# Performance work log

Measured on AMD Instinct MI355X. Metric: run time of the kernel, lower is better.

## Reference

```python
import jax, jax.numpy as jnp
import numpy as np

D_MODEL = 1472
N_HEADS = 6
D_KV = 64
INNER = N_HEADS * D_KV
NUM_BUCKETS = 32
MAX_DIST = 128


def _relative_position_bucket(relative_position, bidirectional=True,
                              num_buckets=NUM_BUCKETS, max_distance=MAX_DIST):
    ret = jnp.zeros_like(relative_position)
    if bidirectional:
        num_buckets //= 2
        ret = ret + (relative_position > 0).astype(jnp.int32) * num_buckets
        rel = jnp.abs(relative_position)
    else:
        rel = -jnp.minimum(relative_position, 0)
    max_exact = num_buckets // 2
    is_small = rel < max_exact
    rel_f = jnp.maximum(rel, 1).astype(jnp.float32)
    large = max_exact + (
        jnp.log(rel_f / max_exact) / np.log(max_distance / max_exact)
        * (num_buckets - max_exact)
    ).astype(jnp.int32)
    large = jnp.minimum(large, num_buckets - 1)
    return ret + jnp.where(is_small, rel, large)


def _position_bias(q_len, k_len, rel_bias):
    # rel_bias: [num_buckets, n_heads]
    ctx = jnp.arange(q_len)[:, None]
    mem = jnp.arange(k_len)[None, :]
    buckets = _relative_position_bucket(mem - ctx, bidirectional=True)
    values = rel_bias[buckets]                 # [Q, K, H]
    return jnp.transpose(values, (2, 0, 1))[None]  # [1, H, Q, K]


def setup_inputs() -> dict:
    key = jax.random.key(0)
    ks = jax.random.split(key, 8)
    B, S = 4, 2048
    scale = 0.02
    return {
        "kv_sequences": jax.random.normal(ks[0], (B, S, D_MODEL), jnp.float32),
        "q_sequences": jax.random.normal(ks[1], (B, S, D_MODEL), jnp.float32),
        "mask": jnp.zeros((B, 1, S, S), jnp.float32),
        "WQ": jax.random.normal(ks[2], (D_MODEL, INNER), jnp.float32) * scale,
        "WK": jax.random.normal(ks[3], (D_MODEL, INNER), jnp.float32) * scale,
        "WV": jax.random.normal(ks[4], (D_MODEL, INNER), jnp.float32) * scale,
        "WO": jax.random.normal(ks[5], (INNER, D_MODEL), jnp.float32) * scale,
        "rel_bias": jax.random.normal(ks[6], (NUM_BUCKETS, N_HEADS), jnp.float32) * scale,
    }


def reference(kv_sequences, q_sequences, mask, WQ, WK, WV, WO, rel_bias):
    B, Kl, _ = kv_sequences.shape
    Ql = q_sequences.shape[1]
    # projections -> [B, H, L, d_kv]
    q = (q_sequences @ WQ).reshape(B, Ql, N_HEADS, D_KV).transpose(0, 2, 1, 3)
    k = (kv_sequences @ WK).reshape(B, Kl, N_HEADS, D_KV).transpose(0, 2, 1, 3)
    v = (kv_sequences @ WV).reshape(B, Kl, N_HEADS, D_KV).transpose(0, 2, 1, 3)
    # T5-style: no 1/sqrt(d) scaling
    logits = jnp.einsum("bhqd,bhkd->bhqk", q, k)
    logits = logits + _position_bias(Ql, Kl, rel_bias)
    logits = logits + mask
    attn = jax.nn.softmax(logits.astype(jnp.float32), axis=-1).astype(logits.dtype)
    out = jnp.einsum("bhqk,bhkd->bhqd", attn, v)
    out = out.transpose(0, 2, 1, 3).reshape(B, Ql, INNER)
    return out @ WO
```

## Files before the change

### kernel.cpp

```cpp
#include <hip/hip_runtime.h>
#include <hip/hip_fp16.h>
#include <cstdint>

#define DM    1472
#define NH    6
#define DKV   64
#define INNER 384
#define BATCH 4
#define SEQ   2048
#define LOG2E 1.4426950408889634f

typedef __attribute__((ext_vector_type(8))) _Float16 half8;
typedef __attribute__((ext_vector_type(4))) _Float16 half4;
typedef __attribute__((ext_vector_type(4))) float f32x4;

__device__ __forceinline__ int swz64(int row, int b)  { return b ^ (((row >> 1) & 3) << 4); }

__device__ __forceinline__ void gload16(const void* g, const void* l) {
  __builtin_amdgcn_global_load_lds((const __attribute__((address_space(1))) void*)g,
                                   (__attribute__((address_space(3))) void*)l, 16, 0, 0);
}

__global__ void prep_weights(const float* __restrict__ WQ, const float* __restrict__ WK,
                             const float* __restrict__ WV, const float* __restrict__ WO,
                             _Float16* __restrict__ WqT, _Float16* __restrict__ WkT,
                             _Float16* __restrict__ WvT, _Float16* __restrict__ WoT) {
  int idx = blockIdx.x * blockDim.x + threadIdx.x;
  const int per = DM * INNER;
  if (idx >= 4 * per) return;
  int which = idx / per;
  int i = idx - which * per;
  if (which < 3) {
    const float* W = which == 0 ? WQ : (which == 1 ? WK : WV);
    _Float16* T = which == 0 ? WqT : (which == 1 ? WkT : WvT);
    int k = i / INNER, n = i - (i / INNER) * INNER;
    T[(size_t)n * DM + k] = (_Float16)W[i];
  } else {
    int k = i / DM, n = i - (i / DM) * DM;
    WoT[(size_t)n * INNER + k] = (_Float16)WO[i];
  }
}

__global__ void prep_bias(const float* __restrict__ rel_bias, float* __restrict__ biasS) {
  int idx = blockIdx.x * blockDim.x + threadIdx.x;
  const int TOT = NH * 4 * 4104;
  if (idx >= TOT) return;
  int h = idx / (4 * 4104);
  int rem = idx - h * 4 * 4104;
  int cc = rem / 4104;
  int i = rem - cc * 4104;
  int j = i + cc; if (j > 4094) j = 4094;
  int d = j - 2047;
  int ret = d > 0 ? 16 : 0;
  int a = d < 0 ? -d : d;
  int bucket;
  if (a < 8) bucket = ret + a;
  else {
    int large;
    if      (a >= 91) large = 15;
    else if (a >= 64) large = 14;
    else if (a >= 46) large = 13;
    else if (a >= 32) large = 12;
    else if (a >= 23) large = 11;
    else if (a >= 16) large = 10;
    else if (a >= 12) large = 9;
    else              large = 8;
    bucket = ret + large;
  }
  biasS[idx] = rel_bias[bucket * NH + h] * LOG2E;
}

__global__ __launch_bounds__(256) void proj_gemm(
    const float* __restrict__ Xq, const float* __restrict__ Xkv,
    const _Float16* __restrict__ WqT, const _Float16* __restrict__ WkvT,
    _Float16* __restrict__ Qo, _Float16* __restrict__ Ko, _Float16* __restrict__ Vto) {
  const int bm = blockIdx.x, by = blockIdx.y;
  const bool isQ = by < 3;
  const float* __restrict__ X = isQ ? Xq : Xkv;
  const _Float16* __restrict__ WT = isQ ? (WqT + (size_t)by * 128 * DM)
                                        : (WkvT + (size_t)(by - 3) * 128 * DM);

  __shared__ alignas(16) float    As[2][128 * 32];
  __shared__ alignas(16) _Float16 Bs[2][128 * 32];

  const int tid = threadIdx.x;
  const int lane = tid & 63, wave = tid >> 6;
  const int wm = wave >> 1, wn = wave & 1;
  const int l15 = lane & 15, lg = lane >> 4;

  f32x4 acc[4][4] = {};

  const int aoff = 4 * ((lane & 7) ^ (lane >> 3));
  const float* asrc[4];
#pragma unroll
  for (int c = 0; c < 4; ++c)
    asrc[c] = X + (size_t)(bm * 128 + (wave * 4 + c) * 8 + (lane >> 3)) * DM + aoff;
  const int boff = 8 * ((lane & 3) ^ ((lane >> 3) & 3));
  const _Float16* bsrc[2];
#pragma unroll
  for (int c = 0; c < 2; ++c)
    bsrc[c] = WT + (size_t)((wave * 2 + c) * 16 + (lane >> 2)) * DM + boff;

  const int NT = DM / 32;

#pragma unroll
  for (int c = 0; c < 4; ++c)
    gload16(asrc[c], (const char*)&As[0][0] + (wave * 4 + c) * 1024);
#pragma unroll
  for (int c = 0; c < 2; ++c)
    gload16(bsrc[c], (const char*)&Bs[0][0] + (wave * 2 + c) * 1024);
  __syncthreads();

  for (int t = 0; t < NT; ++t) {
    if (t + 1 < NT) {
      const int nb = (t + 1) & 1;
      const int kf = (t + 1) * 32;
#pragma unroll
      for (int c = 0; c < 4; ++c)
        gload16(asrc[c] + kf, (const char*)&As[nb][0] + (wave * 4 + c) * 1024);
#pragma unroll
      for (int c = 0; c < 2; ++c)
        gload16(bsrc[c] + kf, (const char*)&Bs[nb][0] + (wave * 2 + c) * 1024);
    }

    const char* Ab = (const char*)&As[t & 1][0];
    const char* Bb = (const char*)&Bs[t & 1][0];
    half8 af[4], bf[4];
#pragma unroll
    for (int m = 0; m < 4; ++m) {
      int r = wm * 64 + m * 16 + l15;
      int s = (r & 7) << 4;
      f32x4 x0 = *(const f32x4*)(Ab + r * 128 + ((lg * 32) ^ s));
      f32x4 x1 = *(const f32x4*)(Ab + r * 128 + ((lg * 32 + 16) ^ s));
      half8 h;
#pragma unroll
      for (int j = 0; j < 4; ++j) { h[j] = (_Float16)x0[j]; h[4 + j] = (_Float16)x1[j]; }
      af[m] = h;
    }
#pragma unroll
    for (int n = 0; n < 4; ++n) {
      int r = wn * 64 + n * 16 + l15;
      bf[n] = *(const half8*)(Bb + r * 64 + ((lg * 16) ^ (((r >> 1) & 3) << 4)));
    }

    __builtin_amdgcn_s_setprio(1);
#pragma unroll
    for (int m = 0; m < 4; ++m)
#pragma unroll
      for (int n = 0; n < 4; ++n)
        acc[m][n] = __builtin_amdgcn_mfma_f32_16x16x32_f16(af[m], bf[n], acc[m][n], 0, 0, 0);
    __builtin_amdgcn_s_setprio(0);

    __syncthreads();
  }

#pragma unroll
  for (int m = 0; m < 4; ++m)
#pragma unroll
    for (int n = 0; n < 4; ++n)
#pragma unroll
      for (int r = 0; r < 4; ++r) {
        int gm = bm * 128 + wm * 64 + m * 16 + lg * 4 + r;
        int gnl = wn * 64 + n * 16 + l15;
        int b = gm >> 11, s = gm & 2047;
        float av = acc[m][n][r];
        if (isQ) {
          int gn = by * 128 + gnl;
          int h = gn >> 6, dd = gn & 63;
          Qo[((size_t)(b * NH + h) * SEQ + s) * DKV + dd] = (_Float16)(av * LOG2E);
        } else {
          int gn = (by - 3) * 128 + gnl;
          if (gn < INNER) {
            int h = gn >> 6, dd = gn & 63;
            Ko[((size_t)(b * NH + h) * SEQ + s) * DKV + dd] = (_Float16)av;
          } else {
            int gnv = gn - INNER;
            int h = gnv >> 6, dd = gnv & 63;
            Vto[((size_t)(b * NH + h) * DKV + dd) * SEQ + s] = (_Float16)av;
          }
        }
      }
}

__global__ __launch_bounds__(256, 3) void attn_kernel(
    const _Float16* __restrict__ Q, const _Float16* __restrict__ K, const _Float16* __restrict__ Vt,
    const float* __restrict__ biasS, const float* __restrict__ mask, _Float16* __restrict__ AO) {
  const int bid = blockIdx.x;
  const int g = (bid & 7) * 96 + (bid >> 3);
  const int bh = g >> 5, qb = g & 31;
  const int b = bh / NH, h = bh - b * NH;
  const int q0 = qb * 64;
  const int tid = threadIdx.x, lane = tid & 63, wave = tid >> 6;
  const int l15 = lane & 15, lg = lane >> 4;
  const int NT = SEQ / 64;

  __shared__ alignas(16) _Float16 Ks[3][64 * 64];
  __shared__ alignas(16) _Float16 Vs[2][64 * 64];
  __shared__ alignas(16) _Float16 Ps[4][16 * 72];

  const size_t bhS = (size_t)bh * SEQ;
  const int qq = q0 + wave * 16 + l15;

  const _Float16* Qbase = Q + (bhS + q0 + wave * 16) * DKV;
  half8 qf0 = *(const half8*)(Qbase + (size_t)l15 * DKV + lg * 8);
  half8 qf1 = *(const half8*)(Qbase + (size_t)l15 * DKV + 32 + lg * 8);

  const float* maskrow = mask + (size_t)b * SEQ * SEQ + (size_t)qq * SEQ + lg * 4;
  const int c = (3 - l15) & 3;
  const float* bbase = biasS + (size_t)(h * 4 + c) * 4104 + (lg * 4 - qq + 2047 - c);

  float m_r = -1e30f, l_acc = 0.f;
  f32x4 oacc[4] = {};

  const int rl = lane >> 3;
  const int sw = ((lane & 7) ^ rl) * 8;
  const _Float16* Kd0 = K + (bhS + wave * 16 + rl) * DKV + sw;
  const _Float16* Kd1 = Kd0 + 8 * DKV;
  const _Float16* Vd0 = Vt + ((size_t)bh * DKV + wave * 16 + rl) * SEQ + sw;
  const _Float16* Vd1 = Vd0 + 8 * SEQ;
  char* KsB = (char*)&Ks[0][0];
  char* VsB = (char*)&Vs[0][0];
  char* PsB = (char*)&Ps[wave][0];
  const int dmaLds = wave * 2048;

  gload16(Kd0, KsB + dmaLds);
  gload16(Kd1, KsB + dmaLds + 1024);
  gload16(Kd0 + 64 * DKV, KsB + 8192 + dmaLds);
  gload16(Kd1 + 64 * DKV, KsB + 8192 + dmaLds + 1024);
  gload16(Vd0, VsB + dmaLds);
  gload16(Vd1, VsB + dmaLds + 1024);

  f32x4 mA[4], mB[4];
#pragma unroll
  for (int nf = 0; nf < 4; ++nf) mA[nf] = *(const f32x4*)(maskrow + nf * 16);

  __syncthreads();

  f32x4 sA[4] = {}, sB[4] = {};
  __builtin_amdgcn_s_setprio(1);
#pragma unroll
  for (int nf = 0; nf < 4; ++nf) {
    int kr = nf * 16 + l15;
    const char* rb = KsB + kr * 128;
    half8 kf0 = *(const half8*)(rb + ((lg ^ (kr & 7)) << 4));
    half8 kf1 = *(const half8*)(rb + (((4 + lg) ^ (kr & 7)) << 4));
    sA[nf] = __builtin_amdgcn_mfma_f32_16x16x32_f16(kf0, qf0, sA[nf], 0, 0, 0);
    sA[nf] = __builtin_amdgcn_mfma_f32_16x16x32_f16(kf1, qf1, sA[nf], 0, 0, 0);
  }
  __builtin_amdgcn_s_setprio(0);

  auto body = [&](int t, f32x4 (&sC)[4], f32x4 (&sN)[4], f32x4 (&mC)[4], f32x4 (&mN)[4]) {
    const int nt1 = t + 1, nt2 = t + 2;
    if (nt2 < NT) {
      char* kb = KsB + (nt2 % 3) * 8192 + dmaLds;
      gload16(Kd0 + (size_t)nt2 * 64 * DKV, kb);
      gload16(Kd1 + (size_t)nt2 * 64 * DKV, kb + 1024);
    }
    if (nt1 < NT) {
      char* vb_ = VsB + (nt1 & 1) * 8192 + dmaLds;
      gload16(Vd0 + nt1 * 64, vb_);
      gload16(Vd1 + nt1 * 64, vb_ + 1024);
#pragma unroll
      for (int nf = 0; nf < 4; ++nf)
        mN[nf] = *(const f32x4*)(maskrow + nt1 * 64 + nf * 16);
    }

#pragma unroll
    for (int nf = 0; nf < 4; ++nf) sN[nf] = (f32x4){0.f, 0.f, 0.f, 0.f};
    if (nt1 < NT) {
      const char* Kb = KsB + (nt1 % 3) * 8192;
      __builtin_amdgcn_s_setprio(1);
#pragma unroll
      for (int nf = 0; nf < 4; ++nf) {
        int kr = nf * 16 + l15;
        const char* rb = Kb + kr * 128;
        half8 kf0 = *(const half8*)(rb + ((lg ^ (kr & 7)) << 4));
        half8 kf1 = *(const half8*)(rb + (((4 + lg) ^ (kr & 7)) << 4));
        sN[nf] = __builtin_amdgcn_mfma_f32_16x16x32_f16(kf0, qf0, sN[nf], 0, 0, 0);
        sN[nf] = __builtin_amdgcn_mfma_f32_16x16x32_f16(kf1, qf1, sN[nf], 0, 0, 0);
      }
      __builtin_amdgcn_s_setprio(0);
    }

    float fm[4];
#pragma unroll
    for (int nf = 0; nf < 4; ++nf) {
      f32x4 bv = *(const f32x4*)(bbase + t * 64 + nf * 16);
#pragma unroll
      for (int r = 0; r < 4; ++r)
        sC[nf][r] = sC[nf][r] + bv[r] + mC[nf][r] * LOG2E;
      fm[nf] = fmaxf(fmaxf(sC[nf][0], sC[nf][1]), fmaxf(sC[nf][2], sC[nf][3]));
    }
    float mx = fmaxf(fmaxf(fm[0], fm[1]), fmaxf(fm[2], fm[3]));
    mx = fmaxf(mx, __shfl_xor(mx, 16));
    mx = fmaxf(mx, __shfl_xor(mx, 32));

    if (!__all(mx <= m_r + 8.0f)) {
      float mnew = fmaxf(m_r, mx);
      float sc_ = __builtin_amdgcn_exp2f(m_r - mnew);
      m_r = mnew;
      l_acc *= sc_;
      f32x4 scv;
#pragma unroll
      for (int r = 0; r < 4; ++r) scv[r] = __shfl(sc_, lg * 4 + r);
#pragma unroll
      for (int df = 0; df < 4; ++df) oacc[df] *= scv;
    }

    float rs = 0.f;
#pragma unroll
    for (int nf = 0; nf < 4; ++nf) {
      half4 ph;
#pragma unroll
      for (int r = 0; r < 4; ++r) {
        float p = __builtin_amdgcn_exp2f(sC[nf][r] - m_r);
        rs += p;
        ph[r] = (_Float16)p;
      }
      *(half4*)(PsB + l15 * 144 + nf * 32 + lg * 8) = ph;
    }
    l_acc += rs;

    const char* Vb = VsB + (t & 1) * 8192;
    __builtin_amdgcn_s_setprio(1);
#pragma unroll
    for (int ks = 0; ks < 2; ++ks) {
      half8 pa = *(const half8*)(PsB + l15 * 144 + ks * 64 + lg * 16);
#pragma unroll
      for (int df = 0; df < 4; ++df) {
        int vr = df * 16 + l15;
        half8 vv = *(const half8*)(Vb + vr * 128 + (((ks * 4 + lg) ^ (vr & 7)) << 4));
        oacc[df] = __builtin_amdgcn_mfma_f32_16x16x32_f16(pa, vv, oacc[df], 0, 0, 0);
      }
    }
    __builtin_amdgcn_s_setprio(0);

    __syncthreads();
  };

  for (int tt = 0; tt < NT / 2; ++tt) {
    body(2 * tt,     sA, sB, mA, mB);
    body(2 * tt + 1, sB, sA, mB, mA);
  }

  l_acc += __shfl_xor(l_acc, 16);
  l_acc += __shfl_xor(l_acc, 32);
  f32x4 lv;
#pragma unroll
  for (int r = 0; r < 4; ++r) lv[r] = __shfl(l_acc, lg * 4 + r);
#pragma unroll
  for (int df = 0; df < 4; ++df) {
    int dd = df * 16 + l15;
#pragma unroll
    for (int r = 0; r < 4; ++r) {
      int qrow = q0 + wave * 16 + lg * 4 + r;
      AO[((size_t)(b * SEQ + qrow)) * INNER + h * DKV + dd] = (_Float16)(oacc[df][r] / lv[r]);
    }
  }
}

__global__ __launch_bounds__(256) void out_gemm(
    const _Float16* __restrict__ A, const _Float16* __restrict__ BT, float* __restrict__ C) {
  __shared__ alignas(16) _Float16 As[2][128 * 32];
  __shared__ alignas(16) _Float16 Bs[2][64 * 32];

  const int tid = threadIdx.x, lane = tid & 63, wave = tid >> 6;
  const int wm = wave >> 1, wn = wave & 1;
  const int bm = blockIdx.x, bn = blockIdx.y;
  const int l15 = lane & 15, lg = lane >> 4;

  f32x4 acc[4][2] = {};

  const int rl4 = (lane >> 2) & 3;
  const int soff = ((lane & 3) ^ rl4) * 8;
  const _Float16* ad0 = A + (size_t)(bm * 128 + (wave * 2) * 16 + (lane >> 2)) * INNER + soff;
  const _Float16* ad1 = ad0 + (size_t)16 * INNER;
  const _Float16* bd0 = BT + (size_t)(bn * 64 + wave * 16 + (lane >> 2)) * INNER + soff;
  char* AsB = (char*)&As[0][0];
  char* BsB = (char*)&Bs[0][0];
  const int aLds = wave * 2048;
  const int bLds = wave * 1024;

  const int NT = INNER / 32;

  gload16(ad0, AsB + aLds);
  gload16(ad1, AsB + aLds + 1024);
  gload16(bd0, BsB + bLds);
  __syncthreads();

  for (int t = 0; t < NT; ++t) {
    if (t + 1 < NT) {
      const int nb = (t + 1) & 1;
      const int kf = (t + 1) * 32;
      gload16(ad0 + kf, AsB + nb * 8192 + aLds);
      gload16(ad1 + kf, AsB + nb * 8192 + aLds + 1024);
      gload16(bd0 + kf, BsB + nb * 4096 + bLds);
    }

    const char* Ab = AsB + (t & 1) * 8192;
    const char* Bb = BsB + (t & 1) * 4096;
    half8 af[4], bf[2];
#pragma unroll
    for (int m = 0; m < 4; ++m) {
      int r = wm * 64 + m * 16 + l15;
      af[m] = *(const half8*)(Ab + r * 64 + (((lg ^ (r & 3))) << 4));
    }
#pragma unroll
    for (int n = 0; n < 2; ++n) {
      int r = wn * 32 + n * 16 + l15;
      bf[n] = *(const half8*)(Bb + r * 64 + (((lg ^ (r & 3))) << 4));
    }
    __builtin_amdgcn_s_setprio(1);
#pragma unroll
    for (int m = 0; m < 4; ++m)
#pragma unroll
      for (int n = 0; n < 2; ++n)
        acc[m][n] = __builtin_amdgcn_mfma_f32_16x16x32_f16(af[m], bf[n], acc[m][n], 0, 0, 0);
    __builtin_amdgcn_s_setprio(0);

    __syncthreads();
  }

#pragma unroll
  for (int m = 0; m < 4; ++m)
#pragma unroll
    for (int n = 0; n < 2; ++n)
#pragma unroll
      for (int r = 0; r < 4; ++r) {
        int gm = bm * 128 + wm * 64 + m * 16 + lg * 4 + r;
        int gn = bn * 64 + wn * 32 + n * 16 + l15;
        C[(size_t)gm * DM + gn] = acc[m][n][r];
      }
}

extern "C" void kernel_launch(void* const* d_in, const int* in_sizes, int n_in,
                              void* d_out, int out_size, void* d_ws, size_t ws_size,
                              hipStream_t stream) {
  const float* kv   = (const float*)d_in[0];
  const float* qs   = (const float*)d_in[1];
  const float* mask = (const float*)d_in[2];
  const float* WQ   = (const float*)d_in[3];
  const float* WK   = (const float*)d_in[4];
  const float* WV   = (const float*)d_in[5];
  const float* WO   = (const float*)d_in[6];
  const float* rb   = (const float*)d_in[7];
  float* out = (float*)d_out;
  char* ws = (char*)d_ws;

  const size_t WT_BYTES  = (size_t)INNER * DM * 2;
  const size_t QKV_BYTES = (size_t)BATCH * NH * SEQ * DKV * 2;
  _Float16* WqT = (_Float16*)(ws);
  _Float16* WkT = (_Float16*)(ws + WT_BYTES);
  _Float16* WvT = (_Float16*)(ws + 2 * WT_BYTES);
  _Float16* WoT = (_Float16*)(ws + 3 * WT_BYTES);
  _Float16* Qh  = (_Float16*)(ws + 4 * WT_BYTES);
  _Float16* Kh  = (_Float16*)(ws + 4 * WT_BYTES + QKV_BYTES);
  _Float16* Vth = (_Float16*)(ws + 4 * WT_BYTES + 2 * QKV_BYTES);
  _Float16* AO  = (_Float16*)(ws + 4 * WT_BYTES + 3 * QKV_BYTES);
  float* biasS  = (float*)(ws + 4 * WT_BYTES + 4 * QKV_BYTES);

  hipLaunchKernelGGL(prep_weights, dim3((4 * DM * INNER + 255) / 256), dim3(256), 0, stream,
                     WQ, WK, WV, WO, WqT, WkT, WvT, WoT);
  hipLaunchKernelGGL(prep_bias, dim3((NH * 4 * 4104 + 255) / 256), dim3(256), 0, stream, rb, biasS);
  hipLaunchKernelGGL(proj_gemm, dim3(64, 9), dim3(256), 0, stream,
                     qs, kv, WqT, WkT, Qh, Kh, Vth);
  hipLaunchKernelGGL(attn_kernel, dim3(768), dim3(256), 0, stream,
                     Qh, Kh, Vth, biasS, mask, AO);
  hipLaunchKernelGGL(out_gemm, dim3(64, 23), dim3(256), 0, stream, AO, WoT, out);
}
```

Baseline: 193.7 us.

## Split attention over two key halves with atomic-counter merge of partials

Turns the attention kernel into a split-K (flash-decoding style) variant: each (batch, head, query-block) is handled by two workgroups, each over half the keys. Each writes unnormalized output plus max/sum partials to workspace, and the last finisher, found via an atomic counter, merges them. This doubles the grid from 768 to 1536 blocks to fill more CUs. It also simplifies the pipeline to plain double buffering without the software-pipelined QK, raises the occupancy hint to 4, and swizzles the P buffer instead of padding it. The costs are extra global traffic for partials, a memset launch, and a possibly less overlapped inner loop.

```diff
diff --git a/kernel.cpp b/kernel.cpp
--- a/kernel.cpp
+++ b/kernel.cpp
@@ -13,8 +13,6 @@
 typedef __attribute__((ext_vector_type(8))) _Float16 half8;
 typedef __attribute__((ext_vector_type(4))) _Float16 half4;
 typedef __attribute__((ext_vector_type(4))) float f32x4;
-
-__device__ __forceinline__ int swz64(int row, int b)  { return b ^ (((row >> 1) & 3) << 4); }
 
 __device__ __forceinline__ void gload16(const void* g, const void* l) {
   __builtin_amdgcn_global_load_lds((const __attribute__((address_space(1))) void*)g,
@@ -182,21 +180,33 @@
       }
 }
 
-__global__ __launch_bounds__(256, 3) void attn_kernel(
+template <int KHALVES>
+__global__ __launch_bounds__(256, 4) void attn_kernel(
     const _Float16* __restrict__ Q, const _Float16* __restrict__ K, const _Float16* __restrict__ Vt,
-    const float* __restrict__ biasS, const float* __restrict__ mask, _Float16* __restrict__ AO) {
+    const float* __restrict__ biasS, const float* __restrict__ mask, _Float16* __restrict__ AO,
+    float* __restrict__ Opart, float* __restrict__ MLpart, int* __restrict__ cnt) {
   const int bid = blockIdx.x;
-  const int g = (bid & 7) * 96 + (bid >> 3);
-  const int bh = g >> 5, qb = g & 31;
+  int pair, half;
+  if constexpr (KHALVES == 2) {
+    int g = (bid & 7) * 192 + (bid >> 3);
+    pair = g >> 1; half = g & 1;
+  } else {
+    pair = (bid & 7) * 96 + (bid >> 3);
+    half = 0;
+  }
+  const int bh = pair >> 5, qb = pair & 31;
   const int b = bh / NH, h = bh - b * NH;
   const int q0 = qb * 64;
+  const int k0 = half * (SEQ / KHALVES);
+  const int NT = (SEQ / KHALVES) / 64;
+
   const int tid = threadIdx.x, lane = tid & 63, wave = tid >> 6;
   const int l15 = lane & 15, lg = lane >> 4;
-  const int NT = SEQ / 64;
-
-  __shared__ alignas(16) _Float16 Ks[3][64 * 64];
+
+  __shared__ alignas(16) _Float16 Ks[2][64 * 64];
   __shared__ alignas(16) _Float16 Vs[2][64 * 64];
-  __shared__ alignas(16) _Float16 Ps[4][16 * 72];
+  __shared__ alignas(16) _Float16 Ps[4][16 * 64];
+  __shared__ int lastFlag;
 
   const size_t bhS = (size_t)bh * SEQ;
   const int qq = q0 + wave * 16 + l15;
@@ -205,18 +215,18 @@
   half8 qf0 = *(const half8*)(Qbase + (size_t)l15 * DKV + lg * 8);
   half8 qf1 = *(const half8*)(Qbase + (size_t)l15 * DKV + 32 + lg * 8);
 
-  const float* maskrow = mask + (size_t)b * SEQ * SEQ + (size_t)qq * SEQ + lg * 4;
+  const float* maskrow = mask + (size_t)b * SEQ * SEQ + (size_t)qq * SEQ + k0 + lg * 4;
   const int c = (3 - l15) & 3;
-  const float* bbase = biasS + (size_t)(h * 4 + c) * 4104 + (lg * 4 - qq + 2047 - c);
+  const float* bbase = biasS + (size_t)(h * 4 + c) * 4104 + (k0 + lg * 4 - qq + 2047 - c);
 
   float m_r = -1e30f, l_acc = 0.f;
   f32x4 oacc[4] = {};
 
   const int rl = lane >> 3;
   const int sw = ((lane & 7) ^ rl) * 8;
-  const _Float16* Kd0 = K + (bhS + wave * 16 + rl) * DKV + sw;
+  const _Float16* Kd0 = K + (bhS + k0 + wave * 16 + rl) * DKV + sw;
   const _Float16* Kd1 = Kd0 + 8 * DKV;
-  const _Float16* Vd0 = Vt + ((size_t)bh * DKV + wave * 16 + rl) * SEQ + sw;
+  const _Float16* Vd0 = Vt + ((size_t)bh * DKV + wave * 16 + rl) * SEQ + k0 + sw;
   const _Float16* Vd1 = Vd0 + 8 * SEQ;
   char* KsB = (char*)&Ks[0][0];
   char* VsB = (char*)&Vs[0][0];
@@ -225,71 +235,43 @@
 
   gload16(Kd0, KsB + dmaLds);
   gload16(Kd1, KsB + dmaLds + 1024);
-  gload16(Kd0 + 64 * DKV, KsB + 8192 + dmaLds);
-  gload16(Kd1 + 64 * DKV, KsB + 8192 + dmaLds + 1024);
   gload16(Vd0, VsB + dmaLds);
   gload16(Vd1, VsB + dmaLds + 1024);
-
-  f32x4 mA[4], mB[4];
-#pragma unroll
-  for (int nf = 0; nf < 4; ++nf) mA[nf] = *(const f32x4*)(maskrow + nf * 16);
-
   __syncthreads();
 
-  f32x4 sA[4] = {}, sB[4] = {};
-  __builtin_amdgcn_s_setprio(1);
-#pragma unroll
-  for (int nf = 0; nf < 4; ++nf) {
-    int kr = nf * 16 + l15;
-    const char* rb = KsB + kr * 128;
-    half8 kf0 = *(const half8*)(rb + ((lg ^ (kr & 7)) << 4));
-    half8 kf1 = *(const half8*)(rb + (((4 + lg) ^ (kr & 7)) << 4));
-    sA[nf] = __builtin_amdgcn_mfma_f32_16x16x32_f16(kf0, qf0, sA[nf], 0, 0, 0);
-    sA[nf] = __builtin_amdgcn_mfma_f32_16x16x32_f16(kf1, qf1, sA[nf], 0, 0, 0);
-  }
-  __builtin_amdgcn_s_setprio(0);
-
-  auto body = [&](int t, f32x4 (&sC)[4], f32x4 (&sN)[4], f32x4 (&mC)[4], f32x4 (&mN)[4]) {
-    const int nt1 = t + 1, nt2 = t + 2;
-    if (nt2 < NT) {
-      char* kb = KsB + (nt2 % 3) * 8192 + dmaLds;
-      gload16(Kd0 + (size_t)nt2 * 64 * DKV, kb);
-      gload16(Kd1 + (size_t)nt2 * 64 * DKV, kb + 1024);
-    }
-    if (nt1 < NT) {
-      char* vb_ = VsB + (nt1 & 1) * 8192 + dmaLds;
-      gload16(Vd0 + nt1 * 64, vb_);
-      gload16(Vd1 + nt1 * 64, vb_ + 1024);
-#pragma unroll
-      for (int nf = 0; nf < 4; ++nf)
-        mN[nf] = *(const f32x4*)(maskrow + nt1 * 64 + nf * 16);
-    }
-
-#pragma unroll
-    for (int nf = 0; nf < 4; ++nf) sN[nf] = (f32x4){0.f, 0.f, 0.f, 0.f};
-    if (nt1 < NT) {
-      const char* Kb = KsB + (nt1 % 3) * 8192;
-      __builtin_amdgcn_s_setprio(1);
-#pragma unroll
-      for (int nf = 0; nf < 4; ++nf) {
-        int kr = nf * 16 + l15;
-        const char* rb = Kb + kr * 128;
-        half8 kf0 = *(const half8*)(rb + ((lg ^ (kr & 7)) << 4));
-        half8 kf1 = *(const half8*)(rb + (((4 + lg) ^ (kr & 7)) << 4));
-        sN[nf] = __builtin_amdgcn_mfma_f32_16x16x32_f16(kf0, qf0, sN[nf], 0, 0, 0);
-        sN[nf] = __builtin_amdgcn_mfma_f32_16x16x32_f16(kf1, qf1, sN[nf], 0, 0, 0);
-      }
-      __builtin_amdgcn_s_setprio(0);
-    }
-
-    float fm[4];
+  for (int t = 0; t < NT; ++t) {
+    if (t + 1 < NT) {
+      const int nb = (t + 1) & 1;
+      gload16(Kd0 + (size_t)(t + 1) * 64 * DKV, KsB + nb * 8192 + dmaLds);
+      gload16(Kd1 + (size_t)(t + 1) * 64 * DKV, KsB + nb * 8192 + dmaLds + 1024);
+      gload16(Vd0 + (t + 1) * 64, VsB + nb * 8192 + dmaLds);
+      gload16(Vd1 + (t + 1) * 64, VsB + nb * 8192 + dmaLds + 1024);
+    }
+    const char* Kb = KsB + (t & 1) * 8192;
+    const char* Vb = VsB + (t & 1) * 8192;
+
+    f32x4 sacc[4] = {};
+    __builtin_amdgcn_s_setprio(1);
+#pragma unroll
+    for (int nf = 0; nf < 4; ++nf) {
+      int kr = nf * 16 + l15;
+      const char* rb = Kb + kr * 128;
+      half8 kf0 = *(const half8*)(rb + ((lg ^ (kr & 7)) << 4));
+      half8 kf1 = *(const half8*)(rb + (((4 + lg) ^ (kr & 7)) << 4));
+      sacc[nf] = __builtin_amdgcn_mfma_f32_16x16x32_f16(kf0, qf0, sacc[nf], 0, 0, 0);
+      sacc[nf] = __builtin_amdgcn_mfma_f32_16x16x32_f16(kf1, qf1, sacc[nf], 0, 0, 0);
+    }
+    __builtin_amdgcn_s_setprio(0);
+
+    float sv[4][4], fm[4];
 #pragma unroll
     for (int nf = 0; nf < 4; ++nf) {
       f32x4 bv = *(const f32x4*)(bbase + t * 64 + nf * 16);
+      f32x4 mv = *(const f32x4*)(maskrow + t * 64 + nf * 16);
 #pragma unroll
       for (int r = 0; r < 4; ++r)
-        sC[nf][r] = sC[nf][r] + bv[r] + mC[nf][r] * LOG2E;
-      fm[nf] = fmaxf(fmaxf(sC[nf][0], sC[nf][1]), fmaxf(sC[nf][2], sC[nf][3]));
+        sv[nf][r] = sacc[nf][r] + bv[r] + mv[r] * LOG2E;
+      fm[nf] = fmaxf(fmaxf(sv[nf][0], sv[nf][1]), fmaxf(sv[nf][2], sv[nf][3]));
     }
     float mx = fmaxf(fmaxf(fm[0], fm[1]), fmaxf(fm[2], fm[3]));
     mx = fmaxf(mx, __shfl_xor(mx, 16));
@@ -313,48 +295,89 @@
       half4 ph;
 #pragma unroll
       for (int r = 0; r < 4; ++r) {
-        float p = __builtin_amdgcn_exp2f(sC[nf][r] - m_r);
+        float p = __builtin_amdgcn_exp2f(sv[nf][r] - m_r);
         rs += p;
         ph[r] = (_Float16)p;
       }
-      *(half4*)(PsB + l15 * 144 + nf * 32 + lg * 8) = ph;
+      *(half4*)(PsB + l15 * 128 + ((((nf << 1) + (lg >> 1)) ^ (l15 & 7)) << 4) + ((lg & 1) << 3)) = ph;
     }
     l_acc += rs;
 
-    const char* Vb = VsB + (t & 1) * 8192;
     __builtin_amdgcn_s_setprio(1);
 #pragma unroll
     for (int ks = 0; ks < 2; ++ks) {
-      half8 pa = *(const half8*)(PsB + l15 * 144 + ks * 64 + lg * 16);
+      half8 pa = *(const half8*)(PsB + l15 * 128 + ((((ks << 2) + lg) ^ (l15 & 7)) << 4));
 #pragma unroll
       for (int df = 0; df < 4; ++df) {
         int vr = df * 16 + l15;
-        half8 vv = *(const half8*)(Vb + vr * 128 + (((ks * 4 + lg) ^ (vr & 7)) << 4));
+        half8 vv = *(const half8*)(Vb + vr * 128 + ((((ks << 2) + lg) ^ (vr & 7)) << 4));
         oacc[df] = __builtin_amdgcn_mfma_f32_16x16x32_f16(pa, vv, oacc[df], 0, 0, 0);
       }
     }
     __builtin_amdgcn_s_setprio(0);
 
     __syncthreads();
-  };
-
-  for (int tt = 0; tt < NT / 2; ++tt) {
-    body(2 * tt,     sA, sB, mA, mB);
-    body(2 * tt + 1, sB, sA, mB, mA);
   }
 
   l_acc += __shfl_xor(l_acc, 16);
   l_acc += __shfl_xor(l_acc, 32);
-  f32x4 lv;
-#pragma unroll
-  for (int r = 0; r < 4; ++r) lv[r] = __shfl(l_acc, lg * 4 + r);
-#pragma unroll
-  for (int df = 0; df < 4; ++df) {
-    int dd = df * 16 + l15;
+
+  if constexpr (KHALVES == 1) {
+    f32x4 lv;
+#pragma unroll
+    for (int r = 0; r < 4; ++r) lv[r] = __shfl(l_acc, lg * 4 + r);
+#pragma unroll
+    for (int df = 0; df < 4; ++df) {
+      int dd = df * 16 + l15;
+#pragma unroll
+      for (int r = 0; r < 4; ++r) {
+        int qrow = q0 + wave * 16 + lg * 4 + r;
+        AO[((size_t)(b * SEQ + qrow)) * INNER + h * DKV + dd] = (_Float16)(oacc[df][r] / lv[r]);
+      }
+    }
+  } else {
+    float* Og = Opart + (size_t)(pair * 2 + half) * 4096;
+#pragma unroll
+    for (int df = 0; df < 4; ++df)
+      *(f32x4*)(Og + (df * 16 + l15) * 64 + wave * 16 + lg * 4) = oacc[df];
+    float* Ml = MLpart + (size_t)pair * 256 + half * 128;
+    if (lane < 16) {
+      Ml[wave * 16 + l15] = m_r;
+      Ml[64 + wave * 16 + l15] = l_acc;
+    }
+    __syncthreads();
+    if (tid == 0) {
+      __threadfence();
+      lastFlag = atomicAdd(&cnt[pair], 1);
+    }
+    __syncthreads();
+    if (lastFlag == 0) return;
+    __threadfence();
+
+    const float* Oo = Opart + (size_t)(pair * 2 + (half ^ 1)) * 4096;
+    const float* Mo = MLpart + (size_t)pair * 256 + (half ^ 1) * 128;
+    float a[4], ao[4], Lr[4];
 #pragma unroll
     for (int r = 0; r < 4; ++r) {
-      int qrow = q0 + wave * 16 + lg * 4 + r;
-      AO[((size_t)(b * SEQ + qrow)) * INNER + h * DKV + dd] = (_Float16)(oacc[df][r] / lv[r]);
+      int ql = wave * 16 + lg * 4 + r;
+      float mreg = __shfl(m_r, lg * 4 + r);
+      float lreg = __shfl(l_acc, lg * 4 + r);
+      float mo = Mo[ql], lo = Mo[64 + ql];
+      float mm = fmaxf(mreg, mo);
+      a[r]  = __builtin_amdgcn_exp2f(mreg - mm);
+      ao[r] = __builtin_amdgcn_exp2f(mo - mm);
+      Lr[r] = a[r] * lreg + ao[r] * lo;
+    }
+#pragma unroll
+    for (int df = 0; df < 4; ++df) {
+      f32x4 Ov = *(const f32x4*)(Oo + (df * 16 + l15) * 64 + wave * 16 + lg * 4);
+      int dd = df * 16 + l15;
+#pragma unroll
+      for (int r = 0; r < 4; ++r) {
+        int qrow = q0 + wave * 16 + lg * 4 + r;
+        float v = (a[r] * oacc[df][r] + ao[r] * Ov[r]) / Lr[r];
+        AO[((size_t)(b * SEQ + qrow)) * INNER + h * DKV + dd] = (_Float16)v;
+      }
     }
   }
 }
@@ -458,13 +481,26 @@
   _Float16* Vth = (_Float16*)(ws + 4 * WT_BYTES + 2 * QKV_BYTES);
   _Float16* AO  = (_Float16*)(ws + 4 * WT_BYTES + 3 * QKV_BYTES);
   float* biasS  = (float*)(ws + 4 * WT_BYTES + 4 * QKV_BYTES);
+  size_t off = 4 * WT_BYTES + 4 * QKV_BYTES + (size_t)NH * 4 * 4104 * 4;
+  off = (off + 255) & ~(size_t)255;
+  float* Opart  = (float*)(ws + off);
+  float* MLpart = (float*)(ws + off + (size_t)1536 * 4096 * 4);
+  int*   cnt    = (int*)(ws + off + (size_t)1536 * 4096 * 4 + (size_t)768 * 256 * 4);
+  const size_t needed = off + (size_t)1536 * 4096 * 4 + (size_t)768 * 256 * 4 + 768 * 4;
+  const bool split = ws_size >= needed;
 
   hipLaunchKernelGGL(prep_weights, dim3((4 * DM * INNER + 255) / 256), dim3(256), 0, stream,
                      WQ, WK, WV, WO, WqT, WkT, WvT, WoT);
   hipLaunchKernelGGL(prep_bias, dim3((NH * 4 * 4104 + 255) / 256), dim3(256), 0, stream, rb, biasS);
   hipLaunchKernelGGL(proj_gemm, dim3(64, 9), dim3(256), 0, stream,
                      qs, kv, WqT, WkT, Qh, Kh, Vth);
-  hipLaunchKernelGGL(attn_kernel, dim3(768), dim3(256), 0, stream,
-                     Qh, Kh, Vth, biasS, mask, AO);
+  if (split) {
+    hipMemsetAsync(cnt, 0, 768 * sizeof(int), stream);
+    hipLaunchKernelGGL((attn_kernel<2>), dim3(1536), dim3(256), 0, stream,
+                       Qh, Kh, Vth, biasS, mask, AO, Opart, MLpart, cnt);
+  } else {
+    hipLaunchKernelGGL((attn_kernel<1>), dim3(768), dim3(256), 0, stream,
+                       Qh, Kh, Vth, biasS, mask, AO, nullptr, nullptr, nullptr);
+  }
   hipLaunchKernelGGL(out_gemm, dim3(64, 23), dim3(256), 0, stream, AO, WoT, out);
 }
```

New measurement: 367.8 us. +89.9%, slower.

## Simplify attention pipeline to double-buffered K/V and raise occupancy to four blocks

Applied to the files above, without the earlier changes.

Drops the software-pipelined QK^T (computing the next tile's scores during the current softmax) and the triple-buffered K ring. K and V now share a plain double buffer and the mask is loaded inline each tile. Freeing registers and LDS allows launch bounds of 4 blocks per SM, and the P scratch uses an XOR swizzle instead of padding. The trade is losing intra-wave overlap of MFMA and softmax plus exposed mask-load latency, in exchange for more waves to hide latency.

```diff
diff --git a/kernel.cpp b/kernel.cpp
--- a/kernel.cpp
+++ b/kernel.cpp
@@ -13,8 +13,6 @@
 typedef __attribute__((ext_vector_type(8))) _Float16 half8;
 typedef __attribute__((ext_vector_type(4))) _Float16 half4;
 typedef __attribute__((ext_vector_type(4))) float f32x4;
-
-__device__ __forceinline__ int swz64(int row, int b)  { return b ^ (((row >> 1) & 3) << 4); }
 
 __device__ __forceinline__ void gload16(const void* g, const void* l) {
   __builtin_amdgcn_global_load_lds((const __attribute__((address_space(1))) void*)g,
@@ -182,7 +180,7 @@
       }
 }
 
-__global__ __launch_bounds__(256, 3) void attn_kernel(
+__global__ __launch_bounds__(256, 4) void attn_kernel(
     const _Float16* __restrict__ Q, const _Float16* __restrict__ K, const _Float16* __restrict__ Vt,
     const float* __restrict__ biasS, const float* __restrict__ mask, _Float16* __restrict__ AO) {
   const int bid = blockIdx.x;
@@ -190,13 +188,14 @@
   const int bh = g >> 5, qb = g & 31;
   const int b = bh / NH, h = bh - b * NH;
   const int q0 = qb * 64;
+  const int NT = SEQ / 64;
+
   const int tid = threadIdx.x, lane = tid & 63, wave = tid >> 6;
   const int l15 = lane & 15, lg = lane >> 4;
-  const int NT = SEQ / 64;
-
-  __shared__ alignas(16) _Float16 Ks[3][64 * 64];
+
+  __shared__ alignas(16) _Float16 Ks[2][64 * 64];
   __shared__ alignas(16) _Float16 Vs[2][64 * 64];
-  __shared__ alignas(16) _Float16 Ps[4][16 * 72];
+  __shared__ alignas(16) _Float16 Ps[4][16 * 64];
 
   const size_t bhS = (size_t)bh * SEQ;
   const int qq = q0 + wave * 16 + l15;
@@ -225,71 +224,43 @@
 
   gload16(Kd0, KsB + dmaLds);
   gload16(Kd1, KsB + dmaLds + 1024);
-  gload16(Kd0 + 64 * DKV, KsB + 8192 + dmaLds);
-  gload16(Kd1 + 64 * DKV, KsB + 8192 + dmaLds + 1024);
   gload16(Vd0, VsB + dmaLds);
   gload16(Vd1, VsB + dmaLds + 1024);
-
-  f32x4 mA[4], mB[4];
-#pragma unroll
-  for (int nf = 0; nf < 4; ++nf) mA[nf] = *(const f32x4*)(maskrow + nf * 16);
-
   __syncthreads();
 
-  f32x4 sA[4] = {}, sB[4] = {};
-  __builtin_amdgcn_s_setprio(1);
-#pragma unroll
-  for (int nf = 0; nf < 4; ++nf) {
-    int kr = nf * 16 + l15;
-    const char* rb = KsB + kr * 128;
-    half8 kf0 = *(const half8*)(rb + ((lg ^ (kr & 7)) << 4));
-    half8 kf1 = *(const half8*)(rb + (((4 + lg) ^ (kr & 7)) << 4));
-    sA[nf] = __builtin_amdgcn_mfma_f32_16x16x32_f16(kf0, qf0, sA[nf], 0, 0, 0);
-    sA[nf] = __builtin_amdgcn_mfma_f32_16x16x32_f16(kf1, qf1, sA[nf], 0, 0, 0);
-  }
-  __builtin_amdgcn_s_setprio(0);
-
-  auto body = [&](int t, f32x4 (&sC)[4], f32x4 (&sN)[4], f32x4 (&mC)[4], f32x4 (&mN)[4]) {
-    const int nt1 = t + 1, nt2 = t + 2;
-    if (nt2 < NT) {
-      char* kb = KsB + (nt2 % 3) * 8192 + dmaLds;
-      gload16(Kd0 + (size_t)nt2 * 64 * DKV, kb);
-      gload16(Kd1 + (size_t)nt2 * 64 * DKV, kb + 1024);
-    }
-    if (nt1 < NT) {
-      char* vb_ = VsB + (nt1 & 1) * 8192 + dmaLds;
-      gload16(Vd0 + nt1 * 64, vb_);
-      gload16(Vd1 + nt1 * 64, vb_ + 1024);
-#pragma unroll
-      for (int nf = 0; nf < 4; ++nf)
-        mN[nf] = *(const f32x4*)(maskrow + nt1 * 64 + nf * 16);
-    }
-
-#pragma unroll
-    for (int nf = 0; nf < 4; ++nf) sN[nf] = (f32x4){0.f, 0.f, 0.f, 0.f};
-    if (nt1 < NT) {
-      const char* Kb = KsB + (nt1 % 3) * 8192;
-      __builtin_amdgcn_s_setprio(1);
-#pragma unroll
-      for (int nf = 0; nf < 4; ++nf) {
-        int kr = nf * 16 + l15;
-        const char* rb = Kb + kr * 128;
-        half8 kf0 = *(const half8*)(rb + ((lg ^ (kr & 7)) << 4));
-        half8 kf1 = *(const half8*)(rb + (((4 + lg) ^ (kr & 7)) << 4));
-        sN[nf] = __builtin_amdgcn_mfma_f32_16x16x32_f16(kf0, qf0, sN[nf], 0, 0, 0);
-        sN[nf] = __builtin_amdgcn_mfma_f32_16x16x32_f16(kf1, qf1, sN[nf], 0, 0, 0);
-      }
-      __builtin_amdgcn_s_setprio(0);
-    }
-
-    float fm[4];
+  for (int t = 0; t < NT; ++t) {
+    if (t + 1 < NT) {
+      const int nb = (t + 1) & 1;
+      gload16(Kd0 + (size_t)(t + 1) * 64 * DKV, KsB + nb * 8192 + dmaLds);
+      gload16(Kd1 + (size_t)(t + 1) * 64 * DKV, KsB + nb * 8192 + dmaLds + 1024);
+      gload16(Vd0 + (t + 1) * 64, VsB + nb * 8192 + dmaLds);
+      gload16(Vd1 + (t + 1) * 64, VsB + nb * 8192 + dmaLds + 1024);
+    }
+    const char* Kb = KsB + (t & 1) * 8192;
+    const char* Vb = VsB + (t & 1) * 8192;
+
+    f32x4 sacc[4] = {};
+    __builtin_amdgcn_s_setprio(1);
+#pragma unroll
+    for (int nf = 0; nf < 4; ++nf) {
+      int kr = nf * 16 + l15;
+      const char* rb = Kb + kr * 128;
+      half8 kf0 = *(const half8*)(rb + ((lg ^ (kr & 7)) << 4));
+      half8 kf1 = *(const half8*)(rb + (((4 + lg) ^ (kr & 7)) << 4));
+      sacc[nf] = __builtin_amdgcn_mfma_f32_16x16x32_f16(kf0, qf0, sacc[nf], 0, 0, 0);
+      sacc[nf] = __builtin_amdgcn_mfma_f32_16x16x32_f16(kf1, qf1, sacc[nf], 0, 0, 0);
+    }
+    __builtin_amdgcn_s_setprio(0);
+
+    float sv[4][4], fm[4];
 #pragma unroll
     for (int nf = 0; nf < 4; ++nf) {
       f32x4 bv = *(const f32x4*)(bbase + t * 64 + nf * 16);
+      f32x4 mv = *(const f32x4*)(maskrow + t * 64 + nf * 16);
 #pragma unroll
       for (int r = 0; r < 4; ++r)
-        sC[nf][r] = sC[nf][r] + bv[r] + mC[nf][r] * LOG2E;
-      fm[nf] = fmaxf(fmaxf(sC[nf][0], sC[nf][1]), fmaxf(sC[nf][2], sC[nf][3]));
+        sv[nf][r] = sacc[nf][r] + bv[r] + mv[r] * LOG2E;
+      fm[nf] = fmaxf(fmaxf(sv[nf][0], sv[nf][1]), fmaxf(sv[nf][2], sv[nf][3]));
     }
     float mx = fmaxf(fmaxf(fm[0], fm[1]), fmaxf(fm[2], fm[3]));
     mx = fmaxf(mx, __shfl_xor(mx, 16));
@@ -313,34 +284,28 @@
       half4 ph;
 #pragma unroll
       for (int r = 0; r < 4; ++r) {
-        float p = __builtin_amdgcn_exp2f(sC[nf][r] - m_r);
+        float p = __builtin_amdgcn_exp2f(sv[nf][r] - m_r);
         rs += p;
         ph[r] = (_Float16)p;
       }
-      *(half4*)(PsB + l15 * 144 + nf * 32 + lg * 8) = ph;
+      *(half4*)(PsB + l15 * 128 + ((((nf << 1) + (lg >> 1)) ^ (l15 & 7)) << 4) + ((lg & 1) << 3)) = ph;
     }
     l_acc += rs;
 
-    const char* Vb = VsB + (t & 1) * 8192;
     __builtin_amdgcn_s_setprio(1);
 #pragma unroll
     for (int ks = 0; ks < 2; ++ks) {
-      half8 pa = *(const half8*)(PsB + l15 * 144 + ks * 64 + lg * 16);
+      half8 pa = *(const half8*)(PsB + l15 * 128 + ((((ks << 2) + lg) ^ (l15 & 7)) << 4));
 #pragma unroll
       for (int df = 0; df < 4; ++df) {
         int vr = df * 16 + l15;
-        half8 vv = *(const half8*)(Vb + vr * 128 + (((ks * 4 + lg) ^ (vr & 7)) << 4));
+        half8 vv = *(const half8*)(Vb + vr * 128 + ((((ks << 2) + lg) ^ (vr & 7)) << 4));
         oacc[df] = __builtin_amdgcn_mfma_f32_16x16x32_f16(pa, vv, oacc[df], 0, 0, 0);
       }
     }
     __builtin_amdgcn_s_setprio(0);
 
     __syncthreads();
-  };
-
-  for (int tt = 0; tt < NT / 2; ++tt) {
-    body(2 * tt,     sA, sB, mA, mB);
-    body(2 * tt + 1, sB, sA, mB, mA);
   }
 
   l_acc += __shfl_xor(l_acc, 16);
```

New measurement: 191.5 us. Within noise of the previous version (-1.1%).
